# Performance work log

Hardware: AMD Instinct MI355X
Metric: run time of the kernel (lower is better)

Reference implementation:

```python
import jax, jax.numpy as jnp
import numpy as np

N = 100000      # total nodes = B_GRAPHS * NODES_PER_GRAPH
NPG = 1000      # nodes per graph (num_nodes in module)
B_GRAPHS = 100
H = 128         # hidden_channels
CIN = 3         # in_channels
E = 1600000     # edges (avg_degree 16)
OUT = 2         # out_channels


def setup_inputs() -> dict:
    key = jax.random.key(0)
    ks = jax.random.split(key, 20)
    s = 0.05
    inp = {
        "x": jax.random.normal(ks[0], (N, CIN), jnp.float32),
        "edge_index": jnp.stack([
            jax.random.randint(ks[1], (E,), 0, N),
            jax.random.randint(ks[2], (E,), 0, N),
        ]).astype(jnp.int64),
        "batch": jnp.repeat(jnp.arange(B_GRAPHS), NPG).astype(jnp.int64),
        # DiffusionConv layer 0: CIN -> H ; layer 1: H -> H
        "W_self0": jax.random.normal(ks[3], (CIN, H), jnp.float32) * s,
        "W_nbr0": jax.random.normal(ks[4], (CIN, H), jnp.float32) * s,
        "b0": jnp.zeros((H,), jnp.float32),
        "W_self1": jax.random.normal(ks[5], (H, H), jnp.float32) * s,
        "W_nbr1": jax.random.normal(ks[6], (H, H), jnp.float32) * s,
        "b1": jnp.zeros((H,), jnp.float32),
        # 2 stacked LSTMs (torch layout: W_ih [4H, in], W_hh [4H, H])
        "Wih0": jax.random.normal(ks[7], (4 * H, H), jnp.float32) * s,
        "Whh0": jax.random.normal(ks[8], (4 * H, H), jnp.float32) * s,
        "bih0": jnp.zeros((4 * H,), jnp.float32),
        "bhh0": jnp.zeros((4 * H,), jnp.float32),
        "Wih1": jax.random.normal(ks[9], (4 * H, H), jnp.float32) * s,
        "Whh1": jax.random.normal(ks[10], (4 * H, H), jnp.float32) * s,
        "bih1": jnp.zeros((4 * H,), jnp.float32),
        "bhh1": jnp.zeros((4 * H,), jnp.float32),
        # output head
        "W_out": jax.random.normal(ks[11], (H, OUT), jnp.float32) * s,
        "b_out": jnp.zeros((OUT,), jnp.float32),
    }
    return inp


def diffusion_conv(h, src, dst, W_self, W_nbr, b):
    # gather-aggregate-transform: out = h W_self + (D^-1 A h) W_nbr + b
    msgs = h[src]                                            # [E, C] gather
    agg = jax.ops.segment_sum(msgs, dst, num_segments=N)     # [N, C] scatter-add
    deg = jax.ops.segment_sum(jnp.ones((src.shape[0], 1), h.dtype), dst,
                              num_segments=N)                # [N, 1]
    agg = agg / jnp.maximum(deg, 1.0)
    return h @ W_self + agg @ W_nbr + b


def lstm_layer(x_seq, Wih, Whh, bih, bhh):
    # x_seq: [T, Bn, H] seq-first, zero initial state (torch default)
    Bn = x_seq.shape[1]
    h0 = jnp.zeros((Bn, H), x_seq.dtype)
    c0 = jnp.zeros((Bn, H), x_seq.dtype)

    def step(carry, xt):
        h, c = carry
        g = xt @ Wih.T + h @ Whh.T + (bih + bhh)   # [Bn, 4H]
        i, f, gg, o = jnp.split(g, 4, axis=-1)     # torch gate order i,f,g,o
        c = jax.nn.sigmoid(f) * c + jax.nn.sigmoid(i) * jnp.tanh(gg)
        h = jax.nn.sigmoid(o) * jnp.tanh(c)
        return (h, c), h

    _, hs = jax.lax.scan(step, (h0, c0), x_seq)
    return hs


def reference(x, edge_index, batch, W_self0, W_nbr0, b0, W_self1, W_nbr1, b1,
              Wih0, Whh0, bih0, bhh0, Wih1, Whh1, bih1, bhh1, W_out, b_out):
    src, dst = edge_index[0], edge_index[1]
    h = jax.nn.relu(diffusion_conv(x, src, dst, W_self0, W_nbr0, b0))
    h = jax.nn.relu(diffusion_conv(h, src, dst, W_self1, W_nbr1, b1))
    # view(-1, num_nodes, hidden): [B_GRAPHS, NPG, H], LSTM seq-first
    seq = h.reshape(B_GRAPHS, NPG, H)
    seq = lstm_layer(seq, Wih0, Whh0, bih0, bhh0)
    seq = lstm_layer(seq, Wih1, Whh1, bih1, bhh1)
    h = seq.reshape(N, H)
    # global_mean_pool over batch vector
    pooled = jax.ops.segment_sum(h, batch, num_segments=B_GRAPHS)
    cnt = jax.ops.segment_sum(jnp.ones((N, 1), h.dtype), batch,
                              num_segments=B_GRAPHS)
    pooled = pooled / jnp.maximum(cnt, 1.0)
    logits = pooled @ W_out + b_out                # [B_GRAPHS, OUT]
    return jax.nn.log_softmax(logits, axis=1)
```

## Files before the change

### kernel.cpp

```cpp
#include <hip/hip_runtime.h>

#define N_NODES 100000
#define NPG     1000
#define B_GR    100
#define HDIM    128
#define E_EDGES 1600000

typedef __attribute__((ext_vector_type(8))) short bf16x8;
typedef __attribute__((ext_vector_type(4))) float f32x4;
typedef unsigned long long u64;
typedef unsigned short u16;

__device__ __forceinline__ float sigf(float x) { return 1.f / (1.f + __expf(-x)); }
__device__ __forceinline__ float tanh_fast(float x) { return 1.f - 2.f / (__expf(2.f * x) + 1.f); }
__device__ __forceinline__ u16 f2bf(float f) {
    unsigned u = __float_as_uint(f);
    unsigned r = (u + 0x7fffu + ((u >> 16) & 1u)) >> 16;
    return (u16)r;
}
__device__ __forceinline__ float bf2f(u16 h) { return __uint_as_float(((unsigned)h) << 16); }
__device__ __forceinline__ f32x4 MF(bf16x8 a, bf16x8 b, f32x4 c) {
    return __builtin_amdgcn_mfma_f32_16x16x32_bf16(a, b, c, 0, 0, 0);
}
__device__ __forceinline__ u64 pack4(f32x4 a) {
    return (u64)f2bf(a[0]) | ((u64)f2bf(a[1]) << 16)
         | ((u64)f2bf(a[2]) << 32) | ((u64)f2bf(a[3]) << 48);
}

__global__ void k_buildx(const int* __restrict__ src, const int* __restrict__ dst,
                         int* __restrict__ cnt, int* __restrict__ ell) {
    int p = blockIdx.x & 7;
    int g = blockIdx.x >> 3;
    int lo = p * 12500, hi = lo + 12500;
    int e1 = (g + 1) * 50000;
    for (int e = g * 50000 + threadIdx.x; e < e1; e += 256) {
        int d = dst[e];
        if (d >= lo && d < hi) {
            int pos = atomicAdd(&cnt[d], 1);
            if (pos < 64) ell[(size_t)d * 64 + pos] = src[e];
        }
    }
}

__global__ __launch_bounds__(256)
void k_conv0w(const float* __restrict__ x, const int* __restrict__ cnt, const int* __restrict__ ell,
              const float* __restrict__ Ws, const float* __restrict__ Wn, const float* __restrict__ b,
              u16* __restrict__ Hbf) {
    int n = blockIdx.x * 4 + (threadIdx.x >> 6);
    int lane = threadIdx.x & 63;
    if (n >= N_NODES) return;
    int degt = cnt[n];
    int deg = min(degt, 64);
    float a0 = 0.f, a1 = 0.f, a2 = 0.f;
    if (lane < deg) {
        int s = ell[(size_t)n * 64 + lane];
        a0 = x[s * 3 + 0]; a1 = x[s * 3 + 1]; a2 = x[s * 3 + 2];
    }
#pragma unroll
    for (int off = 1; off < 64; off <<= 1) {
        a0 += __shfl_xor(a0, off);
        a1 += __shfl_xor(a1, off);
        a2 += __shfl_xor(a2, off);
    }
    float inv = 1.f / fmaxf((float)degt, 1.f);
    a0 *= inv; a1 *= inv; a2 *= inv;
    float x0 = x[n * 3 + 0], x1 = x[n * 3 + 1], x2 = x[n * 3 + 2];
#pragma unroll
    for (int q = 0; q < 2; ++q) {
        int c = lane + 64 * q;
        float acc = b[c]
            + x0 * Ws[c] + x1 * Ws[128 + c] + x2 * Ws[256 + c]
            + a0 * Wn[c] + a1 * Wn[128 + c] + a2 * Wn[256 + c];
        Hbf[(size_t)n * 128 + c] = f2bf(fmaxf(acc, 0.f));
    }
}

__global__ __launch_bounds__(256)
void k_agg2e(const u16* __restrict__ hin, const int* __restrict__ cnt, const int* __restrict__ ell,
             u16* __restrict__ out) {
    int wid = threadIdx.x >> 6;
    int l = threadIdx.x & 63;
    int n = blockIdx.x * 4 + wid;
    if (n >= N_NODES) return;
    int degt = cnt[n];
    int deg = min(degt, 64);
    int myidx = ell[(size_t)n * 64 + l];
    float ax = 0.f, ay = 0.f;
    const unsigned* base = (const unsigned*)hin;
    int j = 0;
    for (; j + 4 <= deg; j += 4) {
        int i0 = __shfl(myidx, j);
        int i1 = __shfl(myidx, j + 1);
        int i2 = __shfl(myidx, j + 2);
        int i3 = __shfl(myidx, j + 3);
        unsigned v0 = base[(size_t)i0 * 64 + l];
        unsigned v1 = base[(size_t)i1 * 64 + l];
        unsigned v2 = base[(size_t)i2 * 64 + l];
        unsigned v3 = base[(size_t)i3 * 64 + l];
        ax += bf2f((u16)v0); ay += bf2f((u16)(v0 >> 16));
        ax += bf2f((u16)v1); ay += bf2f((u16)(v1 >> 16));
        ax += bf2f((u16)v2); ay += bf2f((u16)(v2 >> 16));
        ax += bf2f((u16)v3); ay += bf2f((u16)(v3 >> 16));
    }
    for (; j < deg; ++j) {
        int i0 = __shfl(myidx, j);
        unsigned v = base[(size_t)i0 * 64 + l];
        ax += bf2f((u16)v); ay += bf2f((u16)(v >> 16));
    }
    float dv = fmaxf((float)degt, 1.f);
    unsigned o = (unsigned)f2bf(ax / dv) | ((unsigned)f2bf(ay / dv) << 16);
    *(unsigned*)&out[(size_t)n * 128 + l * 2] = o;
}

__global__ void k_prepc(const float* __restrict__ Wself, const float* __restrict__ Wnbr,
                        u16* __restrict__ WCf) {
    int idx = blockIdx.x * 256 + threadIdx.x;
    int fi = idx & 4095;
    int lo = idx >> 12;
    int lane = fi & 63;
    int colt = (fi >> 6) & 7;
    int kt = fi >> 9;
    int col = colt * 16 + (lane & 15);
    int k0 = kt * 32 + (lane >> 4) * 8;
    u16 o[8];
#pragma unroll
    for (int j = 0; j < 8; ++j) {
        int k = k0 + j;
        float v = (k < 128) ? Wself[k * 128 + col] : Wnbr[(k - 128) * 128 + col];
        u16 hi = f2bf(v);
        o[j] = lo ? f2bf(v - bf2f(hi)) : hi;
    }
    u64* dst = (u64*)(WCf + (size_t)idx * 8);
    dst[0] = (u64)o[0] | ((u64)o[1] << 16) | ((u64)o[2] << 32) | ((u64)o[3] << 48);
    dst[1] = (u64)o[4] | ((u64)o[5] << 16) | ((u64)o[6] << 32) | ((u64)o[7] << 48);
}

__global__ __launch_bounds__(256, 1)
void k_conv1f(const u16* __restrict__ Hbf, const u16* __restrict__ AGbf,
              const u16* __restrict__ WCf, const float* __restrict__ bias,
              u16* __restrict__ Xf) {
    extern __shared__ __align__(16) u16 smem[];
    int tid = threadIdx.x;
    int l = tid & 63, w = tid >> 6;
    {
        const u64* Wsrc = (const u64*)WCf;
        u64* Wd = (u64*)smem;
#pragma unroll
        for (int i = 0; i < 64; ++i)
            Wd[tid + 256 * i] = Wsrc[tid + 256 * i];
    }
    __syncthreads();
    int r0 = blockIdx.x * 256 + w * 64;

#pragma unroll 1
    for (int g = 0; g < 4; ++g) {
        int rowA = r0 + g * 16 + (l & 15);
        int row = min(rowA, N_NODES - 1);
        int koff = (l >> 4) * 8;
        bf16x8 act[8];
#pragma unroll
        for (int kt = 0; kt < 4; ++kt) {
            act[kt]     = *(const bf16x8*)(Hbf  + (size_t)row * 128 + kt * 32 + koff);
            act[4 + kt] = *(const bf16x8*)(AGbf + (size_t)row * 128 + kt * 32 + koff);
        }
        f32x4 acc[8];
#pragma unroll
        for (int c = 0; c < 8; ++c) acc[c] = (f32x4){0.f, 0.f, 0.f, 0.f};
#pragma unroll
        for (int kt = 0; kt < 8; ++kt)
#pragma unroll
            for (int colt = 0; colt < 8; ++colt) {
                bf16x8 wf = *(const bf16x8*)(smem + ((kt * 8 + colt) * 64 + l) * 8);
                acc[colt] = MF(wf, act[kt], acc[colt]);
            }
#pragma unroll
        for (int kt = 0; kt < 8; ++kt)
#pragma unroll
            for (int colt = 0; colt < 8; ++colt) {
                bf16x8 wf = *(const bf16x8*)(smem + 32768 + ((kt * 8 + colt) * 64 + l) * 8);
                acc[colt] = MF(wf, act[kt], acc[colt]);
            }
        if (rowA < N_NODES) {
            int t = rowA / 1000;
            int rv = rowA - t * 1000;
            int rb2 = rv >> 4, rr = rv & 15;
            size_t tilebase = (size_t)(t * 63 + rb2) * 2048 + rr * 8;
#pragma unroll
            for (int colt = 0; colt < 8; ++colt) {
                int col0 = colt * 16 + ((l >> 4) << 2);
                f32x4 v;
#pragma unroll
                for (int reg = 0; reg < 4; ++reg)
                    v[reg] = fmaxf(acc[colt][reg] + bias[col0 + reg], 0.f);
                size_t idx = tilebase + (size_t)((col0 >> 5) * 512 + ((col0 >> 3) & 3) * 128 + (col0 & 7));
                *(u64*)(Xf + idx) = pack4(v);
            }
        }
    }
}

__global__ void k_prepf(const float* __restrict__ Wih0, const float* __restrict__ Whh0,
                        const float* __restrict__ Wih1, const float* __restrict__ Whh1,
                        u16* __restrict__ WTf) {
    int idx = blockIdx.x * 256 + threadIdx.x;
    int lane = idx & 63;
    int gt = (idx >> 6) & 3;
    int kt = (idx >> 8) & 7;
    int w  = (idx >> 11) & 7;
    int l  = idx >> 14;
    int d = 16 * w + (lane & 15);
    int k0 = kt * 32 + (lane >> 4) * 8;
    int wrow = gt * 128 + d;
    const float* Wi = l ? Wih1 : Wih0;
    const float* Wh = l ? Whh1 : Whh0;
    const float* srcp = (k0 < 128) ? (Wi + wrow * 128 + k0) : (Wh + wrow * 128 + (k0 - 128));
    u16 o[8];
#pragma unroll
    for (int j = 0; j < 8; ++j) o[j] = f2bf(srcp[j]);
    u64* dst = (u64*)(WTf + (size_t)idx * 8);
    dst[0] = (u64)o[0] | ((u64)o[1] << 16) | ((u64)o[2] << 32) | ((u64)o[3] << 48);
    dst[1] = (u64)o[4] | ((u64)o[5] << 16) | ((u64)o[6] << 32) | ((u64)o[7] << 48);
}

__global__ void k_bsum(const float* __restrict__ bih0, const float* __restrict__ bhh0,
                       const float* __restrict__ bih1, const float* __restrict__ bhh1,
                       float* __restrict__ bs) {
    int i = blockIdx.x * 256 + threadIdx.x;
    int l = i >> 9, c = i & 511;
    bs[i] = l ? (bih1[c] + bhh1[c]) : (bih0[c] + bhh0[c]);
}

__global__ __launch_bounds__(512, 1)
void k_gemmA(const u16* __restrict__ src, const u16* __restrict__ WTf,
             const float* __restrict__ bsB, u16* __restrict__ Gx, int t0, int layer) {
    extern __shared__ __align__(16) u16 smem[];
    int tid = threadIdx.x;
    int l = tid & 63, w = tid >> 6;
    int rb = blockIdx.x % 63;
    int slice = blockIdx.x / 63;
    {
        const u64* Wsrc = (const u64*)(WTf + (size_t)layer * 131072);
        u64* Wd = (u64*)smem;
#pragma unroll
        for (int i = 0; i < 32; ++i) {
            int j = tid + i * 512;
            int dfrag = j >> 7, r = j & 127;
            int w_ = dfrag >> 4, kt2 = (dfrag >> 2) & 3, gt = dfrag & 3;
            int gfrag = (w_ * 8 + kt2) * 4 + gt;
            Wd[j] = Wsrc[(size_t)gfrag * 128 + r];
        }
    }
    __syncthreads();
    int d = (w << 4) | (l & 15);
    float b0v = bsB[layer * 512 + d];
    float b1v = bsB[layer * 512 + 128 + d];
    float b2v = bsB[layer * 512 + 256 + d];
    float b3v = bsB[layer * 512 + 384 + d];
    const u16* wbase = smem + (size_t)w * 8192 + l * 8;
    for (int tt = 0; tt < 10; ++tt) {
        int t = t0 + slice * 10 + tt;
        const u16* xb = src + ((size_t)t * 63 + rb) * 2048 + l * 8;
        bf16x8 x0 = *(const bf16x8*)(xb);
        bf16x8 x1 = *(const bf16x8*)(xb + 512);
        bf16x8 x2 = *(const bf16x8*)(xb + 1024);
        bf16x8 x3 = *(const bf16x8*)(xb + 1536);
        f32x4 a0 = {b0v, b0v, b0v, b0v};
        f32x4 a1 = {b1v, b1v, b1v, b1v};
        f32x4 a2 = {b2v, b2v, b2v, b2v};
        f32x4 a3 = {b3v, b3v, b3v, b3v};
#pragma unroll
        for (int kt2 = 0; kt2 < 4; ++kt2) {
            bf16x8 xa = (kt2 == 0) ? x0 : (kt2 == 1) ? x1 : (kt2 == 2) ? x2 : x3;
            a0 = MF(xa, *(const bf16x8*)(wbase + (kt2 * 4 + 0) * 512), a0);
            a1 = MF(xa, *(const bf16x8*)(wbase + (kt2 * 4 + 1) * 512), a1);
            a2 = MF(xa, *(const bf16x8*)(wbase + (kt2 * 4 + 2) * 512), a2);
            a3 = MF(xa, *(const bf16x8*)(wbase + (kt2 * 4 + 3) * 512), a3);
        }
        size_t gbase = ((size_t)(t - t0) * 63 + rb) * 8192 + (size_t)w * 1024 + l * 4;
        *(u64*)(Gx + gbase)       = pack4(a0);
        *(u64*)(Gx + gbase + 256) = pack4(a1);
        *(u64*)(Gx + gbase + 512) = pack4(a2);
        *(u64*)(Gx + gbase + 768) = pack4(a3);
    }
}

__global__ __launch_bounds__(512, 1)
void k_recB(const u16* __restrict__ Gx, const u16* __restrict__ WTf,
            u16* __restrict__ H0f, float* __restrict__ pooled,
            u16* __restrict__ hstate, float* __restrict__ cstate,
            int t0, int layer) {
    extern __shared__ __align__(16) u16 smem[];
    u16* Wlds = smem;
    u16* hshA = smem + 65536;
    u16* hshB = smem + 67584;
    int tid = threadIdx.x;
    int l = tid & 63, w = tid >> 6;
    int rb = blockIdx.x;

    {
        u64 hv = (t0 == 0) ? 0ull : ((const u64*)(hstate + (size_t)rb * 2048))[tid];
        ((u64*)hshA)[tid] = hv;
    }
    {
        const u64* Wsrc = (const u64*)(WTf + (size_t)layer * 131072);
        u64* Wd = (u64*)Wlds;
#pragma unroll
        for (int i = 0; i < 32; ++i) {
            int j = tid + i * 512;
            int dfrag = j >> 7, r = j & 127;
            int w_ = dfrag >> 4, kt2 = (dfrag >> 2) & 3, gt = dfrag & 3;
            int gfrag = (w_ * 8 + 4 + kt2) * 4 + gt;
            Wd[j] = Wsrc[(size_t)gfrag * 128 + r];
        }
    }
    float cst0, cst1, cst2, cst3;
    if (t0 == 0) {
        cst0 = cst1 = cst2 = cst3 = 0.f;
    } else {
        const f32x4 cv = *(const f32x4*)(cstate + ((size_t)rb * 512 + tid) * 4);
        cst0 = cv[0]; cst1 = cv[1]; cst2 = cv[2]; cst3 = cv[3];
    }
    __syncthreads();

    int d = (w << 4) | (l & 15);
    int ktp = d >> 5, oct = (d >> 3) & 3, boff = d & 7;
    int hbase = ktp * 512 + ((l >> 4) * 4 + 16 * oct) * 8 + boff;
    const u16* wbase = Wlds + (size_t)w * 8192 + l * 8;
    int n0 = rb * 16;
    int nreal = min(16, NPG - n0);
    int cur = 0;

    for (int tt = 0; tt < 50; ++tt) {
        int t = t0 + tt;
        size_t gbase = ((size_t)tt * 63 + rb) * 8192 + (size_t)w * 1024 + l * 4;
        u64 p0 = *(const u64*)(Gx + gbase);
        u64 p1 = *(const u64*)(Gx + gbase + 256);
        u64 p2 = *(const u64*)(Gx + gbase + 512);
        u64 p3 = *(const u64*)(Gx + gbase + 768);

        const u16* hc = cur ? hshB : hshA;
        u16* hn = cur ? hshA : hshB;
        f32x4 a0 = {0.f, 0.f, 0.f, 0.f};
        f32x4 a1 = {0.f, 0.f, 0.f, 0.f};
        f32x4 a2 = {0.f, 0.f, 0.f, 0.f};
        f32x4 a3 = {0.f, 0.f, 0.f, 0.f};
#pragma unroll
        for (int kt2 = 0; kt2 < 4; ++kt2) {
            bf16x8 hf = *(const bf16x8*)(hc + kt2 * 512 + l * 8);
            a0 = MF(hf, *(const bf16x8*)(wbase + (kt2 * 4 + 0) * 512), a0);
            a1 = MF(hf, *(const bf16x8*)(wbase + (kt2 * 4 + 1) * 512), a1);
            a2 = MF(hf, *(const bf16x8*)(wbase + (kt2 * 4 + 2) * 512), a2);
            a3 = MF(hf, *(const bf16x8*)(wbase + (kt2 * 4 + 3) * 512), a3);
        }
        float hsum = 0.f;
#pragma unroll
        for (int reg = 0; reg < 4; ++reg) {
            float gi = a0[reg] + bf2f((u16)(p0 >> (16 * reg)));
            float gf = a1[reg] + bf2f((u16)(p1 >> (16 * reg)));
            float gg = a2[reg] + bf2f((u16)(p2 >> (16 * reg)));
            float go = a3[reg] + bf2f((u16)(p3 >> (16 * reg)));
            float cprev = (reg == 0) ? cst0 : (reg == 1) ? cst1 : (reg == 2) ? cst2 : cst3;
            float c = sigf(gf) * cprev + sigf(gi) * tanh_fast(gg);
            if (reg == 0) cst0 = c; else if (reg == 1) cst1 = c;
            else if (reg == 2) cst2 = c; else cst3 = c;
            float h = sigf(go) * tanh_fast(c);
            u16 hb = f2bf(h);
            hn[hbase + reg * 8] = hb;
            if (layer == 0) {
                H0f[((size_t)t * 63 + rb) * 2048 + hbase + reg * 8] = hb;
            } else {
                int row = (l >> 4) * 4 + reg;
                if (row < nreal) hsum += h;
            }
        }
        if (layer == 1) {
            hsum += __shfl_xor(hsum, 16);
            hsum += __shfl_xor(hsum, 32);
            if ((l >> 4) == 0) atomicAdd(&pooled[t * 128 + d], hsum);
        }
        __syncthreads();
        cur ^= 1;
    }
    ((u64*)(hstate + (size_t)rb * 2048))[tid] = ((const u64*)(cur ? hshB : hshA))[tid];
    f32x4 cv = {cst0, cst1, cst2, cst3};
    *(f32x4*)(cstate + ((size_t)rb * 512 + tid) * 4) = cv;
}

__global__ void k_head(const float* __restrict__ pooled, const float* __restrict__ Wout,
                       const float* __restrict__ bout, float* __restrict__ out) {
    int gi = threadIdx.x;
    if (gi >= B_GR) return;
    float l0 = bout[0], l1 = bout[1];
    for (int d = 0; d < 128; ++d) {
        float p = pooled[gi * 128 + d] / 1000.0f;
        l0 += p * Wout[d * 2 + 0];
        l1 += p * Wout[d * 2 + 1];
    }
    float m = fmaxf(l0, l1);
    float lse = m + logf(__expf(l0 - m) + __expf(l1 - m));
    out[gi * 2 + 0] = l0 - lse;
    out[gi * 2 + 1] = l1 - lse;
}

extern "C" void kernel_launch(void* const* d_in, const int* in_sizes, int n_in,
                              void* d_out, int out_size, void* d_ws, size_t ws_size,
                              hipStream_t stream) {
    const float* x    = (const float*)d_in[0];
    const int*   ei   = (const int*)d_in[1];
    const int*   srcI = ei;
    const int*   dstI = ei + E_EDGES;
    const float* Ws0  = (const float*)d_in[3];
    const float* Wn0  = (const float*)d_in[4];
    const float* b0   = (const float*)d_in[5];
    const float* Ws1  = (const float*)d_in[6];
    const float* Wn1  = (const float*)d_in[7];
    const float* b1   = (const float*)d_in[8];
    const float* Wih0 = (const float*)d_in[9];
    const float* Whh0 = (const float*)d_in[10];
    const float* bih0 = (const float*)d_in[11];
    const float* bhh0 = (const float*)d_in[12];
    const float* Wih1 = (const float*)d_in[13];
    const float* Whh1 = (const float*)d_in[14];
    const float* bih1 = (const float*)d_in[15];
    const float* bhh1 = (const float*)d_in[16];
    const float* Wout = (const float*)d_in[17];
    const float* bout = (const float*)d_in[18];
    float* out = (float*)d_out;

    char* ws = (char*)d_ws;
    int*   cnt    = (int*)(ws + 0);
    int*   ell    = (int*)(ws + 400128);
    u16*   Hbf    = (u16*)(ws + 26000128);
    u16*   AGbf   = (u16*)(ws + 51600128);
    u16*   Xf     = (u16*)(ws + 77414400);
    u16*   WTf    = (u16*)(ws + 103219200);
    float* bsB    = (float*)(ws + 103743488);
    float* pooled = (float*)(ws + 103747584);
    u16*   hstate = (u16*)(ws + 103798784);
    float* cstate = (float*)(ws + 104056832);
    u16*   WCf    = (u16*)(ws + 104572928);
    u16*   H0f    = (u16*)(ws + 0);
    u16*   Gx     = (u16*)(ws + 25804800);

    hipMemsetAsync(cnt, 0, 400128, stream);
    hipMemsetAsync(pooled, 0, B_GR * 128 * sizeof(float), stream);

    k_buildx<<<256, 256, 0, stream>>>(srcI, dstI, cnt, ell);
    k_conv0w<<<N_NODES / 4, 256, 0, stream>>>(x, cnt, ell, Ws0, Wn0, b0, Hbf);
    k_agg2e<<<N_NODES / 4, 256, 0, stream>>>(Hbf, cnt, ell, AGbf);
    k_prepc<<<32, 256, 0, stream>>>(Ws1, Wn1, WCf);

    hipFuncSetAttribute((const void*)k_conv1f, hipFuncAttributeMaxDynamicSharedMemorySize, 131072);
    hipFuncSetAttribute((const void*)k_gemmA,  hipFuncAttributeMaxDynamicSharedMemorySize, 131072);
    hipFuncSetAttribute((const void*)k_recB,   hipFuncAttributeMaxDynamicSharedMemorySize, 139264);

    k_conv1f<<<(N_NODES + 255) / 256, 256, 131072, stream>>>(Hbf, AGbf, WCf, b1, Xf);

    k_prepf<<<128, 256, 0, stream>>>(Wih0, Whh0, Wih1, Whh1, WTf);
    k_bsum<<<4, 256, 0, stream>>>(bih0, bhh0, bih1, bhh1, bsB);

    for (int layer = 0; layer < 2; ++layer) {
        const u16* srcT = layer ? H0f : Xf;
        for (int half = 0; half < 2; ++half) {
            int t0 = half * 50;
            k_gemmA<<<315, 512, 131072, stream>>>(srcT, WTf, bsB, Gx, t0, layer);
            k_recB<<<63, 512, 139264, stream>>>(Gx, WTf, H0f, pooled, hstate, cstate, t0, layer);
        }
    }

    k_head<<<1, 128, 0, stream>>>(pooled, Wout, bout, out);
}
```

Measured before the change: 923.5 us.

## Simplify edge bucketing, rebalance gate GEMM grid, prefetch gates in recurrence

The ELL build now uses one thread per edge across the full grid instead of a partitioned scan over destination ranges, which avoids reading each edge eight times. The input-gate GEMM runs with 252 blocks, each handling 12-13 timesteps, so the grid fits one wave on the device. The recurrent kernel loads the next timestep's precomputed gate values during the current step's MFMAs. It also swaps __syncthreads for a raw waitcnt-plus-barrier that waits only on LDS, not global memory. The unpartitioned build may see more atomic contention and unordered ELL entries, and the lighter barrier relies on global memory not needing to settle at each step.

```diff
diff --git a/kernel.cpp b/kernel.cpp
--- a/kernel.cpp
+++ b/kernel.cpp
@@ -26,20 +26,15 @@
     return (u64)f2bf(a[0]) | ((u64)f2bf(a[1]) << 16)
          | ((u64)f2bf(a[2]) << 32) | ((u64)f2bf(a[3]) << 48);
 }
-
-__global__ void k_buildx(const int* __restrict__ src, const int* __restrict__ dst,
-                         int* __restrict__ cnt, int* __restrict__ ell) {
-    int p = blockIdx.x & 7;
-    int g = blockIdx.x >> 3;
-    int lo = p * 12500, hi = lo + 12500;
-    int e1 = (g + 1) * 50000;
-    for (int e = g * 50000 + threadIdx.x; e < e1; e += 256) {
-        int d = dst[e];
-        if (d >= lo && d < hi) {
-            int pos = atomicAdd(&cnt[d], 1);
-            if (pos < 64) ell[(size_t)d * 64 + pos] = src[e];
-        }
-    }
+#define BAR() asm volatile("s_waitcnt lgkmcnt(0)\n\ts_barrier" ::: "memory")
+
+__global__ void k_build(const int* __restrict__ src, const int* __restrict__ dst,
+                        int* __restrict__ cnt, int* __restrict__ ell) {
+    int e = blockIdx.x * 256 + threadIdx.x;
+    if (e >= E_EDGES) return;
+    int d = dst[e];
+    int pos = atomicAdd(&cnt[d], 1);
+    if (pos < 64) ell[(size_t)d * 64 + pos] = src[e];
 }
 
 __global__ __launch_bounds__(256)
@@ -238,6 +233,8 @@
     int l = tid & 63, w = tid >> 6;
     int rb = blockIdx.x % 63;
     int slice = blockIdx.x / 63;
+    int nt = (slice < 2) ? 13 : 12;
+    int ts = (slice < 2) ? slice * 13 : 26 + (slice - 2) * 12;
     {
         const u64* Wsrc = (const u64*)(WTf + (size_t)layer * 131072);
         u64* Wd = (u64*)smem;
@@ -257,8 +254,9 @@
     float b2v = bsB[layer * 512 + 256 + d];
     float b3v = bsB[layer * 512 + 384 + d];
     const u16* wbase = smem + (size_t)w * 8192 + l * 8;
-    for (int tt = 0; tt < 10; ++tt) {
-        int t = t0 + slice * 10 + tt;
+    for (int tt = 0; tt < nt; ++tt) {
+        int tc = ts + tt;
+        int t = t0 + tc;
         const u16* xb = src + ((size_t)t * 63 + rb) * 2048 + l * 8;
         bf16x8 x0 = *(const bf16x8*)(xb);
         bf16x8 x1 = *(const bf16x8*)(xb + 512);
@@ -276,7 +274,7 @@
             a2 = MF(xa, *(const bf16x8*)(wbase + (kt2 * 4 + 2) * 512), a2);
             a3 = MF(xa, *(const bf16x8*)(wbase + (kt2 * 4 + 3) * 512), a3);
         }
-        size_t gbase = ((size_t)(t - t0) * 63 + rb) * 8192 + (size_t)w * 1024 + l * 4;
+        size_t gbase = ((size_t)tc * 63 + rb) * 8192 + (size_t)w * 1024 + l * 4;
         *(u64*)(Gx + gbase)       = pack4(a0);
         *(u64*)(Gx + gbase + 256) = pack4(a1);
         *(u64*)(Gx + gbase + 512) = pack4(a2);
@@ -330,14 +328,12 @@
     int nreal = min(16, NPG - n0);
     int cur = 0;
 
+    size_t goff = (size_t)w * 1024 + l * 4;
+    const u64* g0p = (const u64*)(Gx + (size_t)rb * 8192 + goff);
+    u64 p0 = g0p[0], p1 = g0p[32], p2 = g0p[64], p3 = g0p[96];
+
     for (int tt = 0; tt < 50; ++tt) {
         int t = t0 + tt;
-        size_t gbase = ((size_t)tt * 63 + rb) * 8192 + (size_t)w * 1024 + l * 4;
-        u64 p0 = *(const u64*)(Gx + gbase);
-        u64 p1 = *(const u64*)(Gx + gbase + 256);
-        u64 p2 = *(const u64*)(Gx + gbase + 512);
-        u64 p3 = *(const u64*)(Gx + gbase + 768);
-
         const u16* hc = cur ? hshB : hshA;
         u16* hn = cur ? hshA : hshB;
         f32x4 a0 = {0.f, 0.f, 0.f, 0.f};
@@ -351,6 +347,11 @@
             a1 = MF(hf, *(const bf16x8*)(wbase + (kt2 * 4 + 1) * 512), a1);
             a2 = MF(hf, *(const bf16x8*)(wbase + (kt2 * 4 + 2) * 512), a2);
             a3 = MF(hf, *(const bf16x8*)(wbase + (kt2 * 4 + 3) * 512), a3);
+        }
+        u64 q0 = 0, q1 = 0, q2 = 0, q3 = 0;
+        if (tt < 49) {
+            const u64* gp = (const u64*)(Gx + ((size_t)(tt + 1) * 63 + rb) * 8192 + goff);
+            q0 = gp[0]; q1 = gp[32]; q2 = gp[64]; q3 = gp[96];
         }
         float hsum = 0.f;
 #pragma unroll
@@ -378,7 +379,8 @@
             hsum += __shfl_xor(hsum, 32);
             if ((l >> 4) == 0) atomicAdd(&pooled[t * 128 + d], hsum);
         }
-        __syncthreads();
+        BAR();
+        p0 = q0; p1 = q1; p2 = q2; p3 = q3;
         cur ^= 1;
     }
     ((u64*)(hstate + (size_t)rb * 2048))[tid] = ((const u64*)(cur ? hshB : hshA))[tid];
@@ -445,7 +447,7 @@
     hipMemsetAsync(cnt, 0, 400128, stream);
     hipMemsetAsync(pooled, 0, B_GR * 128 * sizeof(float), stream);
 
-    k_buildx<<<256, 256, 0, stream>>>(srcI, dstI, cnt, ell);
+    k_build<<<E_EDGES / 256, 256, 0, stream>>>(srcI, dstI, cnt, ell);
     k_conv0w<<<N_NODES / 4, 256, 0, stream>>>(x, cnt, ell, Ws0, Wn0, b0, Hbf);
     k_agg2e<<<N_NODES / 4, 256, 0, stream>>>(Hbf, cnt, ell, AGbf);
     k_prepc<<<32, 256, 0, stream>>>(Ws1, Wn1, WCf);
@@ -463,7 +465,7 @@
         const u16* srcT = layer ? H0f : Xf;
         for (int half = 0; half < 2; ++half) {
             int t0 = half * 50;
-            k_gemmA<<<315, 512, 131072, stream>>>(srcT, WTf, bsB, Gx, t0, layer);
+            k_gemmA<<<252, 512, 131072, stream>>>(srcT, WTf, bsB, Gx, t0, layer);
             k_recB<<<63, 512, 139264, stream>>>(Gx, WTf, H0f, pooled, hstate, cstate, t0, layer);
         }
     }
```

New measurement: 847.7 us. -8.2%, faster.
